# Performance work log

Measured on AMD Instinct MI355X. Metric: run time of the kernel, lower is better.

The kernel has to match this reference:

```python
import jax, jax.numpy as jnp
import numpy as np

FP8_MAX = 448.0  # torch.finfo(torch.float8_e4m3fn).max
FP8_MIN = -448.0


def per_tensor_quantize(t):
    # amax = max(|min|, |max|) over the whole tensor
    amax = jnp.maximum(jnp.abs(jnp.min(t)), jnp.abs(jnp.max(t)))
    scale = FP8_MAX / jnp.clip(amax, 1e-12, None)
    q = jnp.clip(t * scale, FP8_MIN, FP8_MAX).astype(jnp.float8_e4m3fn)
    inv_scale = (1.0 / scale).astype(jnp.float32)
    return q, inv_scale


def setup_inputs() -> dict:
    key = jax.random.key(0)
    k1, k2 = jax.random.split(key)
    B, S, D_IN, D_OUT = 8, 8192, 1024, 1024
    x = jax.random.normal(k1, (B, S, D_IN), dtype=jnp.float32)
    w = jax.random.normal(k2, (D_OUT, D_IN), dtype=jnp.float32) * 0.02
    qweight, weight_scale = per_tensor_quantize(w)  # fp8 weight + scalar fp32 scale
    return {"x": x, "qweight": qweight, "weight_scale": weight_scale}


def reference(x, qweight, weight_scale):
    # dynamic per-tensor activation quantization (quantize -> fp8)
    qinput, act_scale = per_tensor_quantize(x)
    # fp8 gemm with inline dequant scales (manual dequant-linear path, bias=None)
    A = qinput.astype(x.dtype) * act_scale          # [B, S, D_in]
    W = qweight.astype(x.dtype) * weight_scale.astype(x.dtype)  # [D_out, D_in]
    out = jnp.einsum('bsk,nk->bsn', A, W)           # [B, S, D_out]
    return out
```

## Files before the change

kernel.cpp:

```cpp
#include <hip/hip_runtime.h>
#include <hip/hip_fp8.h>
#include <stdint.h>
#include <cmath>

using f32x4  = __attribute__((ext_vector_type(4)))  float;
using f32x16 = __attribute__((ext_vector_type(16))) float;
using i32x4  = __attribute__((ext_vector_type(4)))  int;
using i32x8  = __attribute__((ext_vector_type(8)))  int;

#define FP8MAX 448.0f

__device__ __forceinline__ void gload_lds16(const void* g, void* l) {
  __builtin_amdgcn_global_load_lds(
      (const __attribute__((address_space(1))) unsigned int*)g,
      (__attribute__((address_space(3))) unsigned int*)l,
      16, 0, 0);
}

__device__ __forceinline__ uint8_t to_fp8(float v) {
  __hip_fp8_e4m3 q(fminf(fmaxf(v, -FP8MAX), FP8MAX));
  return q.__x;
}

__global__ void amax_wconv(const float* __restrict__ x, size_t n4,
                           unsigned int* __restrict__ amax_u,
                           const uint8_t* __restrict__ w,
                           uint8_t* __restrict__ qw, int n1) {
  if ((int)blockIdx.x * 1024 < n1) {
    const float* wf = (const float*)w;
    const unsigned short* wh = (const unsigned short*)w;
    int f32ok = 1, bf16ok = 1;
    for (int i = threadIdx.x; i < 4096; i += 256) {
      float v = wf[i];
      if (!(isfinite(v) && fabsf(v) <= FP8MAX)) f32ok = 0;
      else { __hip_fp8_e4m3 qq(v); if ((float)qq != v) f32ok = 0; }
      float hv = __uint_as_float(((unsigned int)wh[i]) << 16);
      if (!(isfinite(hv) && fabsf(hv) <= FP8MAX)) bf16ok = 0;
      else { __hip_fp8_e4m3 qh(hv); if ((float)qh != hv) bf16ok = 0; }
    }
    __shared__ int sf, sb;
    if (threadIdx.x == 0) { sf = 1; sb = 1; }
    __syncthreads();
    if (!f32ok) atomicAnd(&sf, 0);
    if (!bf16ok) atomicAnd(&sb, 0);
    __syncthreads();
    unsigned int f = sf ? 2u : (sb ? 1u : 0u);

    int i0 = (blockIdx.x * 256 + threadIdx.x) * 4;
    if (i0 < n1) {
      uint32_t out;
      if (f == 2) {
        float4 v = *(const float4*)((const float*)w + i0);
        out = (uint32_t)to_fp8(v.x) | ((uint32_t)to_fp8(v.y) << 8) |
              ((uint32_t)to_fp8(v.z) << 16) | ((uint32_t)to_fp8(v.w) << 24);
      } else if (f == 1) {
        ushort4 h = *(const ushort4*)((const unsigned short*)w + i0);
        out = (uint32_t)to_fp8(__uint_as_float(((unsigned int)h.x) << 16)) |
              ((uint32_t)to_fp8(__uint_as_float(((unsigned int)h.y) << 16)) << 8) |
              ((uint32_t)to_fp8(__uint_as_float(((unsigned int)h.z) << 16)) << 16) |
              ((uint32_t)to_fp8(__uint_as_float(((unsigned int)h.w) << 16)) << 24);
      } else {
        out = *(const uint32_t*)(w + i0);
      }
      *(uint32_t*)(qw + i0) = out;
    }
  }

  const float4* x4 = (const float4*)x;
  float m = 0.0f;
  size_t stride = (size_t)gridDim.x * blockDim.x;
  for (size_t i = (size_t)blockIdx.x * blockDim.x + threadIdx.x; i < n4; i += stride) {
    float4 v = x4[i];
    m = fmaxf(m, fmaxf(fmaxf(fabsf(v.x), fabsf(v.y)),
                       fmaxf(fabsf(v.z), fabsf(v.w))));
  }
  #pragma unroll
  for (int off = 32; off > 0; off >>= 1)
    m = fmaxf(m, __shfl_xor(m, off));
  __shared__ float sm[16];
  int wid = threadIdx.x >> 6;
  if ((threadIdx.x & 63) == 0) sm[wid] = m;
  __syncthreads();
  if (threadIdx.x == 0) {
    int nw = blockDim.x >> 6;
    float r = sm[0];
    for (int i = 1; i < nw; i++) r = fmaxf(r, sm[i]);
    atomicMax(amax_u, __float_as_uint(r));
  }
}

__global__ void quant_kernel(const float* __restrict__ x,
                             uint8_t* __restrict__ q,
                             const float* __restrict__ amax_p, size_t n16) {
  float amax = fmaxf(amax_p[0], 1e-12f);
  float scale = FP8MAX / amax;
  const float4* x4 = (const float4*)x;
  uint4* q16 = (uint4*)q;
  size_t stride = (size_t)gridDim.x * blockDim.x;
  for (size_t i = (size_t)blockIdx.x * blockDim.x + threadIdx.x; i < n16; i += stride) {
    uint32_t w[4];
    #pragma unroll
    for (int j = 0; j < 4; j++) {
      float4 v = x4[i * 4 + j];
      w[j] = (uint32_t)to_fp8(v.x * scale) | ((uint32_t)to_fp8(v.y * scale) << 8) |
             ((uint32_t)to_fp8(v.z * scale) << 16) | ((uint32_t)to_fp8(v.w * scale) << 24);
    }
    uint4 o; o.x = w[0]; o.y = w[1]; o.z = w[2]; o.w = w[3];
    q16[i] = o;
  }
}

#define BM 128
#define BN 128
#define BK 64
#define NBUF 3

__global__ __launch_bounds__(256, 3) void gemm_fp8(
    const uint8_t* __restrict__ A,
    const uint8_t* __restrict__ B,
    float* __restrict__ C,
    const float* __restrict__ amax_p,
    const float* __restrict__ wscale_p,
    int M, int N, int K) {
  __shared__ uint8_t ldsA[NBUF][BM * BK];
  __shared__ uint8_t ldsB[NBUF][BN * BK];

  int nwg = gridDim.x;
  int cpx = nwg >> 3;
  int swz = (blockIdx.x & 7) * cpx + (blockIdx.x >> 3);

  int nstrips = N / BN;
  int bm = (swz / nstrips) * BM;
  int bn = (swz % nstrips) * BN;

  int t = threadIdx.x;
  int lane = t & 63;
  int wave = t >> 6;
  int wm = (wave >> 1) * 64;
  int wn = (wave & 1) * 64;

  float amax = fmaxf(amax_p[0], 1e-12f);
  float scale = FP8MAX / amax;
  float s = (1.0f / scale) * wscale_p[0];

  f32x16 acc[2][2] = {};

  const int rt = t >> 2;
  const int ct = t & 3;

  const int lr = lane & 31;
  const int rsw = (lr >> 1) & 3;
  const int kh = lane >> 5;
  const int c0 = ((2 * kh) ^ rsw) << 4;
  const int c1 = ((2 * kh + 1) ^ rsw) << 4;
  int abase[2], bbase[2];
  #pragma unroll
  for (int i = 0; i < 2; i++) abase[i] = (wm + i * 32 + lr) * BK;
  #pragma unroll
  for (int j = 0; j < 2; j++) bbase[j] = (wn + j * 32 + lr) * BK;

  auto stage = [&](int buf, int kt) {
    int k0 = kt * BK;
    #pragma unroll
    for (int p = 0; p < 2; ++p) {
      int r = p * 64 + rt;
      int gc = (ct ^ ((r >> 1) & 3)) * 16;
      gload_lds16(A + (size_t)(bm + r) * K + k0 + gc, &ldsA[buf][p * 4096 + t * 16]);
      gload_lds16(B + (size_t)(bn + r) * K + k0 + gc, &ldsB[buf][p * 4096 + t * 16]);
    }
  };

  const int NT = K / BK;
  stage(0, 0);
  stage(1, 1);

  for (int tt = 0; tt < NT; ++tt) {
    if (tt + 1 < NT) asm volatile("s_waitcnt vmcnt(4)" ::: "memory");
    else             asm volatile("s_waitcnt vmcnt(0)" ::: "memory");
    __builtin_amdgcn_s_barrier();
    __builtin_amdgcn_sched_barrier(0);

    const uint8_t* bA = &ldsA[tt % NBUF][0];
    const uint8_t* bB = &ldsB[tt % NBUF][0];

    i32x8 af[2], bf[2];
    #pragma unroll
    for (int i = 0; i < 2; i++) {
      i32x4 lo = *(const i32x4*)(bA + abase[i] + c0);
      i32x4 hi = *(const i32x4*)(bA + abase[i] + c1);
      af[i] = (i32x8){lo.x, lo.y, lo.z, lo.w, hi.x, hi.y, hi.z, hi.w};
    }
    #pragma unroll
    for (int j = 0; j < 2; j++) {
      i32x4 lo = *(const i32x4*)(bB + bbase[j] + c0);
      i32x4 hi = *(const i32x4*)(bB + bbase[j] + c1);
      bf[j] = (i32x8){lo.x, lo.y, lo.z, lo.w, hi.x, hi.y, hi.z, hi.w};
    }
    if (tt + 2 < NT) stage((tt + 2) % NBUF, tt + 2);
    asm volatile("s_waitcnt lgkmcnt(0)" ::: "memory");
    __builtin_amdgcn_sched_barrier(0);
    __builtin_amdgcn_s_setprio(1);
    #pragma unroll
    for (int i = 0; i < 2; i++)
      #pragma unroll
      for (int j = 0; j < 2; j++)
        acc[i][j] = __builtin_amdgcn_mfma_scale_f32_32x32x64_f8f6f4(
            af[i], bf[j], acc[i][j],
            0 , 0 ,
            0, 0x7f7f7f7f,
            0, 0x7f7f7f7f);
    __builtin_amdgcn_s_setprio(0);
  }

  #pragma unroll
  for (int i = 0; i < 2; i++) {
    #pragma unroll
    for (int j = 0; j < 2; j++) {
      int row0 = bm + wm + i * 32 + ((lane >> 5) << 2);
      int col = bn + wn + j * 32 + (lane & 31);
      #pragma unroll
      for (int r = 0; r < 16; r++) {
        int row = row0 + (r & 3) + ((r >> 2) << 3);
        C[(size_t)row * N + col] = acc[i][j][r] * s;
      }
    }
  }
}

extern "C" void kernel_launch(void* const* d_in, const int* in_sizes, int n_in,
                              void* d_out, int out_size, void* d_ws, size_t ws_size,
                              hipStream_t stream) {
  const float* x = (const float*)d_in[0];
  const uint8_t* wraw = (const uint8_t*)d_in[1];
  const float* wscale = (const float*)d_in[2];
  float* out = (float*)d_out;

  long long in0 = in_sizes[0];
  long long in1 = in_sizes[1];
  double kd = sqrt((double)in0 * (double)in1 / (double)out_size);
  long long K = (long long)(kd + 0.5);
  long long M = in0 / K;
  long long N = in1 / K;

  unsigned int* amax_u = (unsigned int*)d_ws;
  const float* amax_f = (const float*)d_ws;
  uint8_t* qw = (uint8_t*)d_ws + 4096;
  uint8_t* qx = (uint8_t*)d_ws + (2u << 20);

  hipMemsetAsync(d_ws, 0, 4, stream);
  amax_wconv<<<2048, 256, 0, stream>>>(x, (size_t)(in0 / 4), amax_u,
                                       wraw, qw, (int)in1);
  quant_kernel<<<2048, 256, 0, stream>>>(x, qx, amax_f, (size_t)(in0 / 16));

  dim3 grid((unsigned)((M / BM) * (N / BN)));
  gemm_fp8<<<grid, 256, 0, stream>>>(qx, qw, out, amax_f, wscale,
                                     (int)M, (int)N, (int)K);
}
```

Baseline: 260.7 us.

## Fuse activation quantization into GEMM with a 64-row strip resident in LDS

Drops the separate quantize kernel. Each workgroup now loads a 64x1024 fp32 strip of x, quantizes it to fp8 into LDS with an XOR swizzle, and then loops over all N in 256-column chunks, streaming the weight tiles. This removes the fp8 activation write and re-read to global memory and one kernel launch. In exchange the weight loads lose their multi-buffered pipeline (two syncthreads per k-step with no overlap), the B matrix is re-read by every workgroup, the grid shrinks to 1024 larger workgroups, and D=1024 is hardcoded.

```diff
diff --git a/kernel.cpp b/kernel.cpp
--- a/kernel.cpp
+++ b/kernel.cpp
@@ -20,6 +20,11 @@
 __device__ __forceinline__ uint8_t to_fp8(float v) {
   __hip_fp8_e4m3 q(fminf(fmaxf(v, -FP8MAX), FP8MAX));
   return q.__x;
+}
+
+__device__ __forceinline__ uint32_t quant4(float4 v, float s) {
+  return (uint32_t)to_fp8(v.x * s) | ((uint32_t)to_fp8(v.y * s) << 8) |
+         ((uint32_t)to_fp8(v.z * s) << 16) | ((uint32_t)to_fp8(v.w * s) << 24);
 }
 
 __global__ void amax_wconv(const float* __restrict__ x, size_t n4,
@@ -89,139 +94,95 @@
   }
 }
 
-__global__ void quant_kernel(const float* __restrict__ x,
-                             uint8_t* __restrict__ q,
-                             const float* __restrict__ amax_p, size_t n16) {
-  float amax = fmaxf(amax_p[0], 1e-12f);
-  float scale = FP8MAX / amax;
-  const float4* x4 = (const float4*)x;
-  uint4* q16 = (uint4*)q;
-  size_t stride = (size_t)gridDim.x * blockDim.x;
-  for (size_t i = (size_t)blockIdx.x * blockDim.x + threadIdx.x; i < n16; i += stride) {
-    uint32_t w[4];
-    #pragma unroll
-    for (int j = 0; j < 4; j++) {
-      float4 v = x4[i * 4 + j];
-      w[j] = (uint32_t)to_fp8(v.x * scale) | ((uint32_t)to_fp8(v.y * scale) << 8) |
-             ((uint32_t)to_fp8(v.z * scale) << 16) | ((uint32_t)to_fp8(v.w * scale) << 24);
-    }
-    uint4 o; o.x = w[0]; o.y = w[1]; o.z = w[2]; o.w = w[3];
-    q16[i] = o;
-  }
-}
-
-#define BM 128
-#define BN 128
-#define BK 64
-#define NBUF 3
-
-__global__ __launch_bounds__(256, 3) void gemm_fp8(
-    const uint8_t* __restrict__ A,
+#define SROWS 64
+
+__global__ __launch_bounds__(256, 2) void fused_gemm(
+    const float* __restrict__ X,
     const uint8_t* __restrict__ B,
     float* __restrict__ C,
     const float* __restrict__ amax_p,
-    const float* __restrict__ wscale_p,
-    int M, int N, int K) {
-  __shared__ uint8_t ldsA[NBUF][BM * BK];
-  __shared__ uint8_t ldsB[NBUF][BN * BK];
-
-  int nwg = gridDim.x;
-  int cpx = nwg >> 3;
-  int swz = (blockIdx.x & 7) * cpx + (blockIdx.x >> 3);
-
-  int nstrips = N / BN;
-  int bm = (swz / nstrips) * BM;
-  int bn = (swz % nstrips) * BN;
-
-  int t = threadIdx.x;
-  int lane = t & 63;
-  int wave = t >> 6;
-  int wm = (wave >> 1) * 64;
-  int wn = (wave & 1) * 64;
-
-  float amax = fmaxf(amax_p[0], 1e-12f);
-  float scale = FP8MAX / amax;
-  float s = (1.0f / scale) * wscale_p[0];
-
-  f32x16 acc[2][2] = {};
-
-  const int rt = t >> 2;
-  const int ct = t & 3;
+    const float* __restrict__ wscale_p) {
+  __shared__ uint8_t qa[SROWS * 1024];
+  __shared__ uint8_t qb[256 * 64];
+
+  const int t = threadIdx.x;
+  const int lane = t & 63;
+  const int wave = t >> 6;
+
+  const float amax = fmaxf(amax_p[0], 1e-12f);
+  const float scale = FP8MAX / amax;
+  const float s = (1.0f / scale) * wscale_p[0];
+
+  const float4* x4 = (const float4*)(X + (size_t)blockIdx.x * (SROWS * 1024));
+  #pragma unroll 4
+  for (int i = 0; i < 64; ++i) {
+    float4 v = x4[i * 256 + t];
+    uint32_t wq = quant4(v, scale);
+    int swc = (t >> 2) ^ (i & 15);
+    *(uint32_t*)&qa[i * 1024 + swc * 16 + (t & 3) * 4] = wq;
+  }
 
   const int lr = lane & 31;
+  const int kh = lane >> 5;
+  const int x15 = lr & 15;
   const int rsw = (lr >> 1) & 3;
-  const int kh = lane >> 5;
-  const int c0 = ((2 * kh) ^ rsw) << 4;
-  const int c1 = ((2 * kh + 1) ^ rsw) << 4;
-  int abase[2], bbase[2];
-  #pragma unroll
-  for (int i = 0; i < 2; i++) abase[i] = (wm + i * 32 + lr) * BK;
-  #pragma unroll
-  for (int j = 0; j < 2; j++) bbase[j] = (wn + j * 32 + lr) * BK;
-
-  auto stage = [&](int buf, int kt) {
-    int k0 = kt * BK;
-    #pragma unroll
-    for (int p = 0; p < 2; ++p) {
-      int r = p * 64 + rt;
-      int gc = (ct ^ ((r >> 1) & 3)) * 16;
-      gload_lds16(A + (size_t)(bm + r) * K + k0 + gc, &ldsA[buf][p * 4096 + t * 16]);
-      gload_lds16(B + (size_t)(bn + r) * K + k0 + gc, &ldsB[buf][p * 4096 + t * 16]);
-    }
-  };
-
-  const int NT = K / BK;
-  stage(0, 0);
-  stage(1, 1);
-
-  for (int tt = 0; tt < NT; ++tt) {
-    if (tt + 1 < NT) asm volatile("s_waitcnt vmcnt(4)" ::: "memory");
-    else             asm volatile("s_waitcnt vmcnt(0)" ::: "memory");
-    __builtin_amdgcn_s_barrier();
-    __builtin_amdgcn_sched_barrier(0);
-
-    const uint8_t* bA = &ldsA[tt % NBUF][0];
-    const uint8_t* bB = &ldsB[tt % NBUF][0];
-
-    i32x8 af[2], bf[2];
+  const int brow = t >> 2;
+  const int gsw = ((t & 3) ^ ((t >> 3) & 3)) * 16;
+
+  const size_t c_row0 = (size_t)blockIdx.x * SROWS;
+
+  for (int n = 0; n < 4; ++n) {
+    f32x16 acc[2][2] = {};
+    for (int kt = 0; kt < 16; ++kt) {
+      __syncthreads();
+      #pragma unroll
+      for (int p = 0; p < 4; ++p) {
+        int r = brow + p * 64;
+        gload_lds16(B + (size_t)(n * 256 + r) * 1024 + kt * 64 + gsw,
+                    &qb[p * 4096 + t * 16]);
+      }
+      __syncthreads();
+
+      i32x8 af[2], bf[2];
+      #pragma unroll
+      for (int i = 0; i < 2; i++) {
+        const uint8_t* p = &qa[(i * 32 + lr) * 1024];
+        int cb = kt * 4 + kh * 2;
+        i32x4 lo = *(const i32x4*)(p + ((cb    ) ^ x15) * 16);
+        i32x4 hi = *(const i32x4*)(p + ((cb + 1) ^ x15) * 16);
+        af[i] = (i32x8){lo.x, lo.y, lo.z, lo.w, hi.x, hi.y, hi.z, hi.w};
+      }
+      #pragma unroll
+      for (int j = 0; j < 2; j++) {
+        const uint8_t* p = &qb[(wave * 64 + j * 32 + lr) * 64];
+        i32x4 lo = *(const i32x4*)(p + ((2 * kh    ) ^ rsw) * 16);
+        i32x4 hi = *(const i32x4*)(p + ((2 * kh + 1) ^ rsw) * 16);
+        bf[j] = (i32x8){lo.x, lo.y, lo.z, lo.w, hi.x, hi.y, hi.z, hi.w};
+      }
+      __builtin_amdgcn_s_setprio(1);
+      #pragma unroll
+      for (int i = 0; i < 2; i++)
+        #pragma unroll
+        for (int j = 0; j < 2; j++)
+          acc[i][j] = __builtin_amdgcn_mfma_scale_f32_32x32x64_f8f6f4(
+              af[i], bf[j], acc[i][j],
+              0 , 0 ,
+              0, 0x7f7f7f7f,
+              0, 0x7f7f7f7f);
+      __builtin_amdgcn_s_setprio(0);
+    }
+
     #pragma unroll
     for (int i = 0; i < 2; i++) {
-      i32x4 lo = *(const i32x4*)(bA + abase[i] + c0);
-      i32x4 hi = *(const i32x4*)(bA + abase[i] + c1);
-      af[i] = (i32x8){lo.x, lo.y, lo.z, lo.w, hi.x, hi.y, hi.z, hi.w};
-    }
-    #pragma unroll
-    for (int j = 0; j < 2; j++) {
-      i32x4 lo = *(const i32x4*)(bB + bbase[j] + c0);
-      i32x4 hi = *(const i32x4*)(bB + bbase[j] + c1);
-      bf[j] = (i32x8){lo.x, lo.y, lo.z, lo.w, hi.x, hi.y, hi.z, hi.w};
-    }
-    if (tt + 2 < NT) stage((tt + 2) % NBUF, tt + 2);
-    asm volatile("s_waitcnt lgkmcnt(0)" ::: "memory");
-    __builtin_amdgcn_sched_barrier(0);
-    __builtin_amdgcn_s_setprio(1);
-    #pragma unroll
-    for (int i = 0; i < 2; i++)
-      #pragma unroll
-      for (int j = 0; j < 2; j++)
-        acc[i][j] = __builtin_amdgcn_mfma_scale_f32_32x32x64_f8f6f4(
-            af[i], bf[j], acc[i][j],
-            0 , 0 ,
-            0, 0x7f7f7f7f,
-            0, 0x7f7f7f7f);
-    __builtin_amdgcn_s_setprio(0);
-  }
-
-  #pragma unroll
-  for (int i = 0; i < 2; i++) {
-    #pragma unroll
-    for (int j = 0; j < 2; j++) {
-      int row0 = bm + wm + i * 32 + ((lane >> 5) << 2);
-      int col = bn + wn + j * 32 + (lane & 31);
-      #pragma unroll
-      for (int r = 0; r < 16; r++) {
-        int row = row0 + (r & 3) + ((r >> 2) << 3);
-        C[(size_t)row * N + col] = acc[i][j][r] * s;
+      #pragma unroll
+      for (int j = 0; j < 2; j++) {
+        size_t row0 = c_row0 + i * 32 + (kh << 2);
+        int col = n * 256 + wave * 64 + j * 32 + lr;
+        #pragma unroll
+        for (int r = 0; r < 16; r++) {
+          size_t row = row0 + (r & 3) + ((r >> 2) << 3);
+          C[row * 1024 + col] = acc[i][j][r] * s;
+        }
       }
     }
   }
@@ -240,19 +201,14 @@
   double kd = sqrt((double)in0 * (double)in1 / (double)out_size);
   long long K = (long long)(kd + 0.5);
   long long M = in0 / K;
-  long long N = in1 / K;
 
   unsigned int* amax_u = (unsigned int*)d_ws;
   const float* amax_f = (const float*)d_ws;
   uint8_t* qw = (uint8_t*)d_ws + 4096;
-  uint8_t* qx = (uint8_t*)d_ws + (2u << 20);
 
   hipMemsetAsync(d_ws, 0, 4, stream);
   amax_wconv<<<2048, 256, 0, stream>>>(x, (size_t)(in0 / 4), amax_u,
                                        wraw, qw, (int)in1);
-  quant_kernel<<<2048, 256, 0, stream>>>(x, qx, amax_f, (size_t)(in0 / 16));
-
-  dim3 grid((unsigned)((M / BM) * (N / BN)));
-  gemm_fp8<<<grid, 256, 0, stream>>>(qx, qw, out, amax_f, wscale,
-                                     (int)M, (int)N, (int)K);
-}
+  fused_gemm<<<(unsigned)(M / SROWS), 256, 0, stream>>>(x, qw, out,
+                                                        amax_f, wscale);
+}
```

Result: faster. 233.3 us (-10.5%).
